# Performance work log

Measured on AMD Instinct MI355X. Metric: run time of the kernel, lower is better.

The kernel has to match this reference:

```python
import jax, jax.numpy as jnp
import numpy as np

BN_EPS = 1e-5


def conv1x1(x, W, b):
    # x: [B, Cin, N], W: [Cout, Cin], b: [Cout]
    return jnp.einsum('bcn,oc->bon', x, W) + b[None, :, None]


def batchnorm(x, gamma, beta):
    # training-mode BatchNorm1d over (batch, spatial) for x: [B, C, N]
    m = jnp.mean(x, axis=(0, 2), keepdims=True)
    v = jnp.var(x, axis=(0, 2), keepdims=True)
    return (x - m) * jax.lax.rsqrt(v + BN_EPS) * gamma[None, :, None] + beta[None, :, None]


def square_distance(a, b):
    # a: [B, N, 3], b: [B, S, 3] -> [B, N, S]
    aa = jnp.sum(a * a, axis=-1, keepdims=True)        # [B,N,1]
    bb = jnp.sum(b * b, axis=-1)[:, None, :]           # [B,1,S]
    return aa + bb - 2.0 * jnp.einsum('bnc,bsc->bns', a, b)


def setup_inputs() -> dict:
    key = jax.random.key(0)
    ks = jax.random.split(key, 16)
    B, N, S = 4, 8192, 2048
    D1, D2 = 128, 256
    Cin, Cout = D1 + D2, 256
    hid = Cout  # res_expansion = 1.0
    inp = {
        'xyz1': jax.random.normal(ks[0], (B, N, 3), jnp.float32),
        'xyz2': jax.random.normal(ks[1], (B, S, 3), jnp.float32),
        'points1': jax.random.normal(ks[2], (B, D1, N), jnp.float32),
        'points2': jax.random.normal(ks[3], (B, D2, S), jnp.float32),
        # fuse: Conv1d(Cin->Cout,k=1) + BN + ReLU
        'W_fuse': jax.random.normal(ks[4], (Cout, Cin), jnp.float32) * (1.0 / np.sqrt(Cin)),
        'b_fuse': jnp.zeros((Cout,), jnp.float32),
        'g_fuse': jnp.ones((Cout,), jnp.float32),
        'be_fuse': jnp.zeros((Cout,), jnp.float32),
        # extraction residual block: conv1 -> bn -> relu -> conv2 -> bn, +res, relu
        'W1': jax.random.normal(ks[5], (hid, Cout), jnp.float32) * (1.0 / np.sqrt(Cout)),
        'b1': jnp.zeros((hid,), jnp.float32),
        'g1': jnp.ones((hid,), jnp.float32),
        'be1': jnp.zeros((hid,), jnp.float32),
        'W2': jax.random.normal(ks[6], (Cout, hid), jnp.float32) * (1.0 / np.sqrt(hid)),
        'b2': jnp.zeros((Cout,), jnp.float32),
        'g2': jnp.ones((Cout,), jnp.float32),
        'be2': jnp.zeros((Cout,), jnp.float32),
    }
    return inp


def reference(xyz1, xyz2, points1, points2,
              W_fuse, b_fuse, g_fuse, be_fuse,
              W1, b1, g1, be1, W2, b2, g2, be2):
    B, N, _ = xyz1.shape
    p2 = jnp.transpose(points2, (0, 2, 1))  # [B, S, D2]
    # 3-NN inverse-distance interpolation
    dists = square_distance(xyz1, xyz2)                 # [B, N, S]
    neg_d3, idx = jax.lax.top_k(-dists, 3)              # 3 smallest distances
    d3 = -neg_d3                                        # [B, N, 3]
    recip = 1.0 / (d3 + 1e-8)
    weight = recip / jnp.sum(recip, axis=2, keepdims=True)  # [B, N, 3]
    gathered = jax.vmap(lambda pts, i: pts[i])(p2, idx)     # [B, N, 3, D2]
    interp = jnp.sum(gathered * weight[..., None], axis=2)  # [B, N, D2]
    # concat skip features
    p1 = jnp.transpose(points1, (0, 2, 1))              # [B, N, D1]
    new_points = jnp.concatenate([p1, interp], axis=-1) # [B, N, D1+D2]
    x = jnp.transpose(new_points, (0, 2, 1))            # [B, Cin, N]
    # fuse: ConvBNReLU1D
    x = jax.nn.relu(batchnorm(conv1x1(x, W_fuse, b_fuse), g_fuse, be_fuse))
    # extraction: residual ConvBNReLURes1D block
    y = jax.nn.relu(batchnorm(conv1x1(x, W1, b1), g1, be1))
    y = batchnorm(conv1x1(y, W2, b2), g2, be2)
    return jax.nn.relu(x + y)
```

## Files before the change

kernel.cpp:

```cpp
#include <hip/hip_runtime.h>
#include <cstdint>
#include <cstddef>

#define B_ 4
#define N_ 8192
#define S_ 2048
#define M_ 32768

typedef short bf16x8 __attribute__((ext_vector_type(8)));
typedef float f32x4 __attribute__((ext_vector_type(4)));

__device__ __forceinline__ float bf2f(unsigned short u) {
  union { unsigned int i; float f; } v; v.i = ((unsigned int)u) << 16; return v.f;
}
__device__ __forceinline__ unsigned short f2bf(float f) {
  union { float f; unsigned int i; } v; v.f = f;
  return (unsigned short)((v.i + 0x7FFFu + ((v.i >> 16) & 1u)) >> 16);
}

__global__ void pack_weights(const float* __restrict__ Wf, const float* __restrict__ W1,
                             const float* __restrict__ W2, unsigned short* __restrict__ out) {
  int i = blockIdx.x * 256 + threadIdx.x;
  float v;
  if (i < 98304)       v = Wf[i];
  else if (i < 163840) v = W1[i - 98304];
  else                 v = W2[i - 163840];
  out[i] = f2bf(v);
}

__global__ void transpose_to_bf16(const float* __restrict__ src, unsigned short* __restrict__ dst,
                                  int C, int Nsp, int ldo, int coff) {
  __shared__ float t[32][33];
  int b = blockIdx.z;
  int n0 = blockIdx.x * 32, c0 = blockIdx.y * 32;
  int x = threadIdx.x, y = threadIdx.y;
  const float* s = src + ((size_t)b * C + c0) * Nsp + n0;
#pragma unroll
  for (int k = 0; k < 4; ++k)
    t[y + k * 8][x] = s[(size_t)(y + k * 8) * Nsp + x];
  __syncthreads();
#pragma unroll
  for (int k = 0; k < 4; ++k) {
    int n = n0 + y + k * 8;
    dst[((size_t)b * Nsp + n) * ldo + coff + c0 + x] = f2bf(t[x][y + k * 8]);
  }
}

__device__ __forceinline__ bool lexlt(float da, int ia, float db, int ib) {
  return (da < db) || (da == db && ia < ib);
}

__global__ __launch_bounds__(256, 8) void knn_interp_kernel(
    const float* __restrict__ xyz1, const float* __restrict__ xyz2,
    const unsigned short* __restrict__ p2t, unsigned short* __restrict__ np) {
  __shared__ float4 sp[1024];
  __shared__ float sw[16][3];
  __shared__ int   sidx[16][3];
  int t = threadIdx.x;
  int b = blockIdx.y;
  const float* xb = xyz2 + (size_t)b * S_ * 3;

  int lane = t & 63, wave = t >> 6;
  int sub = lane & 15;
  int pib = wave * 4 + (lane >> 4);
  int n = blockIdx.x * 16 + pib;
  const float* q = xyz1 + ((size_t)b * N_ + n) * 3;
  float px = q[0], py = q[1], pz = q[2];
  float nx = -2.f * px, ny = -2.f * py, nz = -2.f * pz;
  float aa = fmaf(px, px, fmaf(py, py, pz * pz));

  float d0 = 1e30f, d1 = 1e30f, d2 = 1e30f;
  int i0 = S_, i1 = S_, i2 = S_;

  for (int chunk = 0; chunk < 2; ++chunk) {
    __syncthreads();
    for (int i = t; i < 1024; i += 256) {
      int c = chunk * 1024 + i;
      float cx = xb[3 * c], cy = xb[3 * c + 1], cz = xb[3 * c + 2];
      sp[i] = make_float4(cx, cy, cz, fmaf(cx, cx, fmaf(cy, cy, cz * cz)));
    }
    __syncthreads();
    int sbase = chunk * 1024;
#pragma unroll 4
    for (int i = 0; i < 64; ++i) {
      int sl = i * 16 + sub;
      float4 c = sp[sl];
      float d = fmaf(nx, c.x, fmaf(ny, c.y, fmaf(nz, c.z, c.w)));
      int s = sbase + sl;
      bool b0 = d < d0, b1 = d < d1, b2 = d < d2;
      d2 = b1 ? d1 : (b2 ? d : d2);
      i2 = b1 ? i1 : (b2 ? s : i2);
      d1 = b0 ? d0 : (b1 ? d : d1);
      i1 = b0 ? i0 : (b1 ? s : i1);
      d0 = b0 ? d : d0;
      i0 = b0 ? s : i0;
    }
  }

#pragma unroll
  for (int m = 1; m <= 8; m <<= 1) {
    float e0 = __shfl_xor(d0, m, 64), e1 = __shfl_xor(d1, m, 64), e2 = __shfl_xor(d2, m, 64);
    int   j0 = __shfl_xor(i0, m, 64), j1 = __shfl_xor(i1, m, 64), j2 = __shfl_xor(i2, m, 64);
    bool l0 = lexlt(d0, i0, e0, j0);
    float m0d = l0 ? d0 : e0;  int m0i = l0 ? i0 : j0;
    float x0d = l0 ? e0 : d0;  int x0i = l0 ? j0 : i0;
    bool l11 = lexlt(d1, i1, e1, j1);
    float n1d = l11 ? d1 : e1; int n1i = l11 ? i1 : j1;
    float y1d = l11 ? e1 : d1; int y1i = l11 ? j1 : i1;
    bool l1 = lexlt(n1d, n1i, x0d, x0i);
    float m1d = l1 ? n1d : x0d; int m1i = l1 ? n1i : x0i;
    bool l01 = lexlt(d0, i0, e1, j1);
    float p1d = l01 ? e1 : d0; int p1i = l01 ? j1 : i0;
    bool l10 = lexlt(d1, i1, e0, j0);
    float p2d = l10 ? e0 : d1; int p2i = l10 ? j0 : i1;
    bool lp = lexlt(p1d, p1i, p2d, p2i);
    float p3d = lp ? p1d : p2d; int p3i = lp ? p1i : p2i;
    bool l22 = lexlt(d2, i2, e2, j2);
    float p4d = l22 ? d2 : e2; int p4i = l22 ? i2 : j2;
    bool l2 = lexlt(p3d, p3i, p4d, p4i);
    float m2d = l2 ? p3d : p4d; int m2i = l2 ? p3i : p4i;
    (void)y1d; (void)y1i;
    d0 = m0d; i0 = m0i; d1 = m1d; i1 = m1i; d2 = m2d; i2 = m2i;
  }

  if (sub == 0) {
    float t0 = aa + d0, t1 = aa + d1, t2 = aa + d2;
    float r0 = 1.f / (t0 + 1e-8f), r1 = 1.f / (t1 + 1e-8f), r2 = 1.f / (t2 + 1e-8f);
    float rs = 1.f / (r0 + r1 + r2);
    sw[pib][0] = r0 * rs; sw[pib][1] = r1 * rs; sw[pib][2] = r2 * rs;
    sidx[pib][0] = i0; sidx[pib][1] = i1; sidx[pib][2] = i2;
  }
  __syncthreads();

  for (int p = wave; p < 16; p += 4) {
    float w0 = sw[p][0], w1 = sw[p][1], w2 = sw[p][2];
    const ushort4* g0 = (const ushort4*)(p2t + ((size_t)b * S_ + sidx[p][0]) * 256) + lane;
    const ushort4* g1 = (const ushort4*)(p2t + ((size_t)b * S_ + sidx[p][1]) * 256) + lane;
    const ushort4* g2 = (const ushort4*)(p2t + ((size_t)b * S_ + sidx[p][2]) * 256) + lane;
    ushort4 a = *g0, c = *g1, e = *g2;
    ushort4 o;
    o.x = f2bf(w0 * bf2f(a.x) + w1 * bf2f(c.x) + w2 * bf2f(e.x));
    o.y = f2bf(w0 * bf2f(a.y) + w1 * bf2f(c.y) + w2 * bf2f(e.y));
    o.z = f2bf(w0 * bf2f(a.z) + w1 * bf2f(c.z) + w2 * bf2f(e.z));
    o.w = f2bf(w0 * bf2f(a.w) + w1 * bf2f(c.w) + w2 * bf2f(e.w));
    int nn = blockIdx.x * 16 + p;
    *((ushort4*)(np + ((size_t)b * N_ + nn) * 384 + 128) + lane) = o;
  }
}

__global__ __launch_bounds__(256) void gemm_bt(const unsigned short* __restrict__ A,
                                               const unsigned short* __restrict__ Bw,
                                               float* __restrict__ C, float* __restrict__ sums,
                                               int K) {
  __shared__ unsigned short As[128 * 64];
  __shared__ unsigned short Bs[128 * 64];
  int tid = threadIdx.x;
  int lane = tid & 63, wave = tid >> 6;
  int wr = wave >> 1, wc = wave & 1;
  size_t m0 = (size_t)blockIdx.x * 128;
  int n0 = blockIdx.y * 128;
  int lr = lane & 15, lk = lane >> 4;
  f32x4 acc[4][4] = {};

  for (int kt = 0; kt < K; kt += 64) {
#pragma unroll
    for (int i = 0; i < 4; ++i) {
      int ch = i * 256 + tid;
      int row = ch >> 3;
      int col = (ch & 7) * 8;
      __builtin_amdgcn_global_load_lds(
          (const __attribute__((address_space(1))) void*)(A + (m0 + row) * K + kt + col),
          (__attribute__((address_space(3))) void*)(As + ch * 8), 16, 0, 0);
    }
#pragma unroll
    for (int i = 0; i < 4; ++i) {
      int ch = i * 256 + tid;
      int row = ch >> 3;
      int col = (ch & 7) * 8;
      __builtin_amdgcn_global_load_lds(
          (const __attribute__((address_space(1))) void*)(Bw + (size_t)(n0 + row) * K + kt + col),
          (__attribute__((address_space(3))) void*)(Bs + ch * 8), 16, 0, 0);
    }
    __syncthreads();

    bf16x8 af[4][2], bf[4][2];
#pragma unroll
    for (int m = 0; m < 4; ++m)
#pragma unroll
      for (int kk = 0; kk < 2; ++kk)
        af[m][kk] = *(const bf16x8*)(As + (wr * 64 + m * 16 + lr) * 64 + kk * 32 + lk * 8);
#pragma unroll
    for (int nn = 0; nn < 4; ++nn)
#pragma unroll
      for (int kk = 0; kk < 2; ++kk)
        bf[nn][kk] = *(const bf16x8*)(Bs + (wc * 64 + nn * 16 + lr) * 64 + kk * 32 + lk * 8);

#pragma unroll
    for (int m = 0; m < 4; ++m)
#pragma unroll
      for (int nn = 0; nn < 4; ++nn)
#pragma unroll
        for (int kk = 0; kk < 2; ++kk)
          acc[m][nn] = __builtin_amdgcn_mfma_f32_16x16x32_bf16(af[m][kk], bf[nn][kk], acc[m][nn], 0, 0, 0);
    __syncthreads();
  }

#pragma unroll
  for (int m = 0; m < 4; ++m) {
    size_t row = m0 + wr * 64 + m * 16 + lk * 4;
#pragma unroll
    for (int j = 0; j < 4; ++j) {
      float* cr = C + (row + j) * 256 + n0 + wc * 64 + lr;
#pragma unroll
      for (int nn = 0; nn < 4; ++nn)
        cr[nn * 16] = acc[m][nn][j];
    }
  }

  float cs[4], cq[4];
#pragma unroll
  for (int nn = 0; nn < 4; ++nn) {
    float s = 0.f, qq = 0.f;
#pragma unroll
    for (int m = 0; m < 4; ++m)
#pragma unroll
      for (int j = 0; j < 4; ++j) { float v = acc[m][nn][j]; s += v; qq = fmaf(v, v, qq); }
    cs[nn] = s; cq[nn] = qq;
  }
#pragma unroll
  for (int off = 16; off <= 32; off <<= 1) {
#pragma unroll
    for (int nn = 0; nn < 4; ++nn) {
      cs[nn] += __shfl_xor(cs[nn], off, 64);
      cq[nn] += __shfl_xor(cq[nn], off, 64);
    }
  }
  if (lk == 0) {
#pragma unroll
    for (int nn = 0; nn < 4; ++nn) {
      int c = n0 + wc * 64 + nn * 16 + lr;
      atomicAdd(&sums[c], cs[nn]);
      atomicAdd(&sums[256 + c], cq[nn]);
    }
  }
}

__global__ void bn_relu_kernel(const float* __restrict__ X, const float* __restrict__ sums,
                               const float* __restrict__ g, const float* __restrict__ be,
                               unsigned short* __restrict__ Y) {
  __shared__ float sc[256], sh[256];
  int t = threadIdx.x;
  {
    float s = sums[t], q = sums[256 + t];
    float m = s * (1.0f / 32768.0f);
    float v = q * (1.0f / 32768.0f) - m * m;
    float scale = g[t] * rsqrtf(v + 1e-5f);
    sc[t] = scale; sh[t] = be[t] - m * scale;
  }
  __syncthreads();
  const float4* X4 = (const float4*)X;
  ushort4* Y4 = (ushort4*)Y;
  for (size_t i = (size_t)blockIdx.x * 256 + t; i < (size_t)M_ * 64; i += 2048 * 256) {
    float4 x = X4[i];
    int c0 = (int)((i * 4) & 255);
    ushort4 o;
    o.x = f2bf(fmaxf(x.x * sc[c0 + 0] + sh[c0 + 0], 0.f));
    o.y = f2bf(fmaxf(x.y * sc[c0 + 1] + sh[c0 + 1], 0.f));
    o.z = f2bf(fmaxf(x.z * sc[c0 + 2] + sh[c0 + 2], 0.f));
    o.w = f2bf(fmaxf(x.w * sc[c0 + 3] + sh[c0 + 3], 0.f));
    Y4[i] = o;
  }
}

__global__ void final_kernel(const float* __restrict__ Z, const unsigned short* __restrict__ Xb,
                             const float* __restrict__ sums2, const float* __restrict__ g2,
                             const float* __restrict__ be2, float* __restrict__ out) {
  __shared__ float sc[64], sh[64];
  __shared__ float tile[64 * 65];
  int t = threadIdx.x;
  int o0 = blockIdx.y * 64;
  if (t < 64) {
    int c = o0 + t;
    float s = sums2[c], q = sums2[256 + c];
    float m = s * (1.0f / 32768.0f);
    float v = q * (1.0f / 32768.0f) - m * m;
    float scale = g2[c] * rsqrtf(v + 1e-5f);
    sc[t] = scale; sh[t] = be2[c] - m * scale;
  }
  __syncthreads();
  size_t m0 = (size_t)blockIdx.x * 64;
  int rl = t >> 4, cq = t & 15;
#pragma unroll
  for (int rr = 0; rr < 4; ++rr) {
    int row = rr * 16 + rl;
    size_t base = (m0 + row) * 256 + o0 + cq * 4;
    float4 z = *(const float4*)(Z + base);
    ushort4 x = *(const ushort4*)(Xb + base);
    int c = cq * 4;
    tile[row * 65 + c + 0] = fmaxf(z.x * sc[c + 0] + sh[c + 0] + bf2f(x.x), 0.f);
    tile[row * 65 + c + 1] = fmaxf(z.y * sc[c + 1] + sh[c + 1] + bf2f(x.y), 0.f);
    tile[row * 65 + c + 2] = fmaxf(z.z * sc[c + 2] + sh[c + 2] + bf2f(x.z), 0.f);
    tile[row * 65 + c + 3] = fmaxf(z.w * sc[c + 3] + sh[c + 3] + bf2f(x.w), 0.f);
  }
  __syncthreads();
  int b = (int)(m0 >> 13);
  int nbase = (int)(m0 & 8191);
  int orow = t >> 4, nq = t & 15;
#pragma unroll
  for (int ov = 0; ov < 4; ++ov) {
    int o = ov * 16 + orow;
    float4 v;
    v.x = tile[(nq * 4 + 0) * 65 + o];
    v.y = tile[(nq * 4 + 1) * 65 + o];
    v.z = tile[(nq * 4 + 2) * 65 + o];
    v.w = tile[(nq * 4 + 3) * 65 + o];
    *(float4*)(out + ((size_t)(b * 256 + o0 + o)) * 8192 + nbase + nq * 4) = v;
  }
}

extern "C" void kernel_launch(void* const* d_in, const int* in_sizes, int n_in,
                              void* d_out, int out_size, void* d_ws, size_t ws_size,
                              hipStream_t stream) {
  const float* xyz1    = (const float*)d_in[0];
  const float* xyz2    = (const float*)d_in[1];
  const float* points1 = (const float*)d_in[2];
  const float* points2 = (const float*)d_in[3];
  const float* W_fuse  = (const float*)d_in[4];
  const float* g_fuse  = (const float*)d_in[6];
  const float* be_fuse = (const float*)d_in[7];
  const float* W1      = (const float*)d_in[8];
  const float* g1      = (const float*)d_in[10];
  const float* be1     = (const float*)d_in[11];
  const float* W2      = (const float*)d_in[12];
  const float* g2      = (const float*)d_in[14];
  const float* be2     = (const float*)d_in[15];
  float* out = (float*)d_out;

  char* ws = (char*)d_ws;
  float* lin = (float*)ws;                   ws += (size_t)M_ * 256 * 4;
  unsigned short* xb = (unsigned short*)ws;  ws += (size_t)M_ * 256 * 2;
  unsigned short* np = (unsigned short*)ws;  ws += (size_t)M_ * 384 * 2;
  unsigned short* yb = np;
  unsigned short* p2t = (unsigned short*)ws; ws += (size_t)B_ * S_ * 256 * 2;
  unsigned short* wb = (unsigned short*)ws;  ws += 229376 * 2;
  float* stats = (float*)ws;

  hipMemsetAsync(stats, 0, 6 * 256 * sizeof(float), stream);
  pack_weights<<<896, 256, 0, stream>>>(W_fuse, W1, W2, wb);
  transpose_to_bf16<<<dim3(256, 4, 4), dim3(32, 8), 0, stream>>>(points1, np, 128, N_, 384, 0);
  transpose_to_bf16<<<dim3(64, 8, 4), dim3(32, 8), 0, stream>>>(points2, p2t, 256, S_, 256, 0);
  knn_interp_kernel<<<dim3(N_ / 16, B_), 256, 0, stream>>>(xyz1, xyz2, p2t, np);
  gemm_bt<<<dim3(M_ / 128, 2), 256, 0, stream>>>(np, wb, lin, stats, 384);
  bn_relu_kernel<<<2048, 256, 0, stream>>>(lin, stats, g_fuse, be_fuse, xb);
  gemm_bt<<<dim3(M_ / 128, 2), 256, 0, stream>>>(xb, wb + 98304, lin, stats + 512, 256);
  bn_relu_kernel<<<2048, 256, 0, stream>>>(lin, stats + 512, g1, be1, yb);
  gemm_bt<<<dim3(M_ / 128, 2), 256, 0, stream>>>(yb, wb + 163840, lin, stats + 1024, 256);
  final_kernel<<<dim3(M_ / 64, 4), 256, 0, stream>>>(lin, xb, stats + 1024, g2, be2, out);
}
```

Measured before the change: 183.0 us.

## Restructure KNN as point-per-lane with candidate split across waves; shrink GEMM M tile

The KNN kernel now gives each lane its own query point, and the 8 waves each scan a 256-candidate slice. The slices are read from a precomputed float4 array (coords plus squared norm) built in the prep kernel, which replaces the per-block LDS staging and the shuffle-based merge. The per-wave top-3 lists are merged through shared memory, and the insertion step uses fmed3/fmin for the distances. The GEMM tile is cut from 128 to 64 rows, doubling the number of blocks. In exchange, the broadcast candidate loads go through the global/scalar cache, and the GEMM reuses each B tile over fewer rows.

```diff
diff --git a/kernel.cpp b/kernel.cpp
--- a/kernel.cpp
+++ b/kernel.cpp
@@ -18,14 +18,21 @@
   return (unsigned short)((v.i + 0x7FFFu + ((v.i >> 16) & 1u)) >> 16);
 }
 
-__global__ void pack_weights(const float* __restrict__ Wf, const float* __restrict__ W1,
-                             const float* __restrict__ W2, unsigned short* __restrict__ out) {
+__global__ void prep_kernel(const float* __restrict__ Wf, const float* __restrict__ W1,
+                            const float* __restrict__ W2, unsigned short* __restrict__ wout,
+                            const float* __restrict__ xyz2, float4* __restrict__ c4) {
   int i = blockIdx.x * 256 + threadIdx.x;
-  float v;
-  if (i < 98304)       v = Wf[i];
-  else if (i < 163840) v = W1[i - 98304];
-  else                 v = W2[i - 163840];
-  out[i] = f2bf(v);
+  if (i < 229376) {
+    float v;
+    if (i < 98304)       v = Wf[i];
+    else if (i < 163840) v = W1[i - 98304];
+    else                 v = W2[i - 163840];
+    wout[i] = f2bf(v);
+  } else {
+    int j = i - 229376;
+    float x = xyz2[3 * j], y = xyz2[3 * j + 1], z = xyz2[3 * j + 2];
+    c4[j] = make_float4(x, y, z, fmaf(x, x, fmaf(y, y, z * z)));
+  }
 }
 
 __global__ void transpose_to_bf16(const float* __restrict__ src, unsigned short* __restrict__ dst,
@@ -50,101 +57,87 @@
   return (da < db) || (da == db && ia < ib);
 }
 
-__global__ __launch_bounds__(256, 8) void knn_interp_kernel(
-    const float* __restrict__ xyz1, const float* __restrict__ xyz2,
+__global__ __launch_bounds__(512, 4) void knn_interp_kernel(
+    const float* __restrict__ xyz1, const float4* __restrict__ c4,
     const unsigned short* __restrict__ p2t, unsigned short* __restrict__ np) {
-  __shared__ float4 sp[1024];
-  __shared__ float sw[16][3];
-  __shared__ int   sidx[16][3];
+  __shared__ float sd[8][64][3];
+  __shared__ int   si[8][64][3];
+  __shared__ float sw[64][3];
+  __shared__ int   sidx[64][3];
   int t = threadIdx.x;
-  int b = blockIdx.y;
-  const float* xb = xyz2 + (size_t)b * S_ * 3;
-
   int lane = t & 63, wave = t >> 6;
-  int sub = lane & 15;
-  int pib = wave * 4 + (lane >> 4);
-  int n = blockIdx.x * 16 + pib;
-  const float* q = xyz1 + ((size_t)b * N_ + n) * 3;
+  int g = blockIdx.x * 64 + lane;
+  int b = (blockIdx.x * 64) >> 13;
+  const float* q = xyz1 + (size_t)g * 3;
   float px = q[0], py = q[1], pz = q[2];
-  float nx = -2.f * px, ny = -2.f * py, nz = -2.f * pz;
   float aa = fmaf(px, px, fmaf(py, py, pz * pz));
+  const float4* cb = c4 + ((size_t)b << 11) + (wave << 8);
+  int base = wave << 8;
 
   float d0 = 1e30f, d1 = 1e30f, d2 = 1e30f;
   int i0 = S_, i1 = S_, i2 = S_;
-
-  for (int chunk = 0; chunk < 2; ++chunk) {
-    __syncthreads();
-    for (int i = t; i < 1024; i += 256) {
-      int c = chunk * 1024 + i;
-      float cx = xb[3 * c], cy = xb[3 * c + 1], cz = xb[3 * c + 2];
-      sp[i] = make_float4(cx, cy, cz, fmaf(cx, cx, fmaf(cy, cy, cz * cz)));
-    }
-    __syncthreads();
-    int sbase = chunk * 1024;
-#pragma unroll 4
-    for (int i = 0; i < 64; ++i) {
-      int sl = i * 16 + sub;
-      float4 c = sp[sl];
-      float d = fmaf(nx, c.x, fmaf(ny, c.y, fmaf(nz, c.z, c.w)));
-      int s = sbase + sl;
-      bool b0 = d < d0, b1 = d < d1, b2 = d < d2;
-      d2 = b1 ? d1 : (b2 ? d : d2);
-      i2 = b1 ? i1 : (b2 ? s : i2);
-      d1 = b0 ? d0 : (b1 ? d : d1);
-      i1 = b0 ? i0 : (b1 ? s : i1);
-      d0 = b0 ? d : d0;
-      i0 = b0 ? s : i0;
-    }
-  }
-
-#pragma unroll
-  for (int m = 1; m <= 8; m <<= 1) {
-    float e0 = __shfl_xor(d0, m, 64), e1 = __shfl_xor(d1, m, 64), e2 = __shfl_xor(d2, m, 64);
-    int   j0 = __shfl_xor(i0, m, 64), j1 = __shfl_xor(i1, m, 64), j2 = __shfl_xor(i2, m, 64);
-    bool l0 = lexlt(d0, i0, e0, j0);
-    float m0d = l0 ? d0 : e0;  int m0i = l0 ? i0 : j0;
-    float x0d = l0 ? e0 : d0;  int x0i = l0 ? j0 : i0;
-    bool l11 = lexlt(d1, i1, e1, j1);
-    float n1d = l11 ? d1 : e1; int n1i = l11 ? i1 : j1;
-    float y1d = l11 ? e1 : d1; int y1i = l11 ? j1 : i1;
-    bool l1 = lexlt(n1d, n1i, x0d, x0i);
-    float m1d = l1 ? n1d : x0d; int m1i = l1 ? n1i : x0i;
-    bool l01 = lexlt(d0, i0, e1, j1);
-    float p1d = l01 ? e1 : d0; int p1i = l01 ? j1 : i0;
-    bool l10 = lexlt(d1, i1, e0, j0);
-    float p2d = l10 ? e0 : d1; int p2i = l10 ? j0 : i1;
-    bool lp = lexlt(p1d, p1i, p2d, p2i);
-    float p3d = lp ? p1d : p2d; int p3i = lp ? p1i : p2i;
-    bool l22 = lexlt(d2, i2, e2, j2);
-    float p4d = l22 ? d2 : e2; int p4i = l22 ? i2 : j2;
-    bool l2 = lexlt(p3d, p3i, p4d, p4i);
-    float m2d = l2 ? p3d : p4d; int m2i = l2 ? p3i : p4i;
-    (void)y1d; (void)y1i;
-    d0 = m0d; i0 = m0i; d1 = m1d; i1 = m1i; d2 = m2d; i2 = m2i;
-  }
-
-  if (sub == 0) {
-    float t0 = aa + d0, t1 = aa + d1, t2 = aa + d2;
+  for (int j = 0; j < 256; j += 8) {
+    float4 cc0 = cb[j + 0], cc1 = cb[j + 1], cc2 = cb[j + 2], cc3 = cb[j + 3];
+    float4 cc4 = cb[j + 4], cc5 = cb[j + 5], cc6 = cb[j + 6], cc7 = cb[j + 7];
+#define KNN_INS(CC, U)                                                        \
+    {                                                                         \
+      float dot = fmaf(px, CC.x, fmaf(py, CC.y, pz * CC.z));                  \
+      float d = fmaf(-2.f, dot, CC.w);                     \
+      int s = base + j + U;                                                   \
+      bool b0 = d < d0, b1 = d < d1, b2 = d < d2;                             \
+      i2 = b1 ? i1 : (b2 ? s : i2);                                           \
+      i1 = b0 ? i0 : (b1 ? s : i1);                                           \
+      i0 = b0 ? s : i0;                                                       \
+      float nd1 = __builtin_amdgcn_fmed3f(d, d0, d1);                         \
+      float nd2 = __builtin_amdgcn_fmed3f(d, d1, d2);                         \
+      d0 = fminf(d0, d);                                                      \
+      d1 = nd1; d2 = nd2;                                                     \
+    }
+    KNN_INS(cc0, 0) KNN_INS(cc1, 1) KNN_INS(cc2, 2) KNN_INS(cc3, 3)
+    KNN_INS(cc4, 4) KNN_INS(cc5, 5) KNN_INS(cc6, 6) KNN_INS(cc7, 7)
+#undef KNN_INS
+  }
+  sd[wave][lane][0] = d0; sd[wave][lane][1] = d1; sd[wave][lane][2] = d2;
+  si[wave][lane][0] = i0; si[wave][lane][1] = i1; si[wave][lane][2] = i2;
+  __syncthreads();
+
+  if (t < 64) {
+    float e0 = sd[0][t][0], e1 = sd[0][t][1], e2 = sd[0][t][2];
+    int   j0 = si[0][t][0], j1 = si[0][t][1], j2 = si[0][t][2];
+#pragma unroll
+    for (int w = 1; w < 8; ++w) {
+#pragma unroll
+      for (int k = 0; k < 3; ++k) {
+        float d = sd[w][t][k];
+        int s = si[w][t][k];
+        bool b0 = lexlt(d, s, e0, j0), b1 = lexlt(d, s, e1, j1), b2 = lexlt(d, s, e2, j2);
+        e2 = b1 ? e1 : (b2 ? d : e2);  j2 = b1 ? j1 : (b2 ? s : j2);
+        e1 = b0 ? e0 : (b1 ? d : e1);  j1 = b0 ? j0 : (b1 ? s : j1);
+        e0 = b0 ? d : e0;              j0 = b0 ? s : j0;
+      }
+    }
+    float t0 = aa + e0, t1 = aa + e1, t2 = aa + e2;
     float r0 = 1.f / (t0 + 1e-8f), r1 = 1.f / (t1 + 1e-8f), r2 = 1.f / (t2 + 1e-8f);
     float rs = 1.f / (r0 + r1 + r2);
-    sw[pib][0] = r0 * rs; sw[pib][1] = r1 * rs; sw[pib][2] = r2 * rs;
-    sidx[pib][0] = i0; sidx[pib][1] = i1; sidx[pib][2] = i2;
-  }
-  __syncthreads();
-
-  for (int p = wave; p < 16; p += 4) {
+    sw[t][0] = r0 * rs; sw[t][1] = r1 * rs; sw[t][2] = r2 * rs;
+    sidx[t][0] = j0; sidx[t][1] = j1; sidx[t][2] = j2;
+  }
+  __syncthreads();
+
+  const unsigned short* pb = p2t + ((size_t)b * S_) * 256;
+  for (int p = wave; p < 64; p += 8) {
     float w0 = sw[p][0], w1 = sw[p][1], w2 = sw[p][2];
-    const ushort4* g0 = (const ushort4*)(p2t + ((size_t)b * S_ + sidx[p][0]) * 256) + lane;
-    const ushort4* g1 = (const ushort4*)(p2t + ((size_t)b * S_ + sidx[p][1]) * 256) + lane;
-    const ushort4* g2 = (const ushort4*)(p2t + ((size_t)b * S_ + sidx[p][2]) * 256) + lane;
+    const ushort4* g0 = (const ushort4*)(pb + (size_t)sidx[p][0] * 256) + lane;
+    const ushort4* g1 = (const ushort4*)(pb + (size_t)sidx[p][1] * 256) + lane;
+    const ushort4* g2 = (const ushort4*)(pb + (size_t)sidx[p][2] * 256) + lane;
     ushort4 a = *g0, c = *g1, e = *g2;
     ushort4 o;
     o.x = f2bf(w0 * bf2f(a.x) + w1 * bf2f(c.x) + w2 * bf2f(e.x));
     o.y = f2bf(w0 * bf2f(a.y) + w1 * bf2f(c.y) + w2 * bf2f(e.y));
     o.z = f2bf(w0 * bf2f(a.z) + w1 * bf2f(c.z) + w2 * bf2f(e.z));
     o.w = f2bf(w0 * bf2f(a.w) + w1 * bf2f(c.w) + w2 * bf2f(e.w));
-    int nn = blockIdx.x * 16 + p;
-    *((ushort4*)(np + ((size_t)b * N_ + nn) * 384 + 128) + lane) = o;
+    size_t g2r = (size_t)blockIdx.x * 64 + p;
+    *((ushort4*)(np + g2r * 384 + 128) + lane) = o;
   }
 }
 
@@ -152,19 +145,19 @@
                                                const unsigned short* __restrict__ Bw,
                                                float* __restrict__ C, float* __restrict__ sums,
                                                int K) {
-  __shared__ unsigned short As[128 * 64];
+  __shared__ unsigned short As[64 * 64];
   __shared__ unsigned short Bs[128 * 64];
   int tid = threadIdx.x;
   int lane = tid & 63, wave = tid >> 6;
   int wr = wave >> 1, wc = wave & 1;
-  size_t m0 = (size_t)blockIdx.x * 128;
+  size_t m0 = (size_t)blockIdx.x * 64;
   int n0 = blockIdx.y * 128;
   int lr = lane & 15, lk = lane >> 4;
-  f32x4 acc[4][4] = {};
+  f32x4 acc[2][4] = {};
 
   for (int kt = 0; kt < K; kt += 64) {
 #pragma unroll
-    for (int i = 0; i < 4; ++i) {
+    for (int i = 0; i < 2; ++i) {
       int ch = i * 256 + tid;
       int row = ch >> 3;
       int col = (ch & 7) * 8;
@@ -183,12 +176,12 @@
     }
     __syncthreads();
 
-    bf16x8 af[4][2], bf[4][2];
-#pragma unroll
-    for (int m = 0; m < 4; ++m)
+    bf16x8 af[2][2], bf[4][2];
+#pragma unroll
+    for (int m = 0; m < 2; ++m)
 #pragma unroll
       for (int kk = 0; kk < 2; ++kk)
-        af[m][kk] = *(const bf16x8*)(As + (wr * 64 + m * 16 + lr) * 64 + kk * 32 + lk * 8);
+        af[m][kk] = *(const bf16x8*)(As + (wr * 32 + m * 16 + lr) * 64 + kk * 32 + lk * 8);
 #pragma unroll
     for (int nn = 0; nn < 4; ++nn)
 #pragma unroll
@@ -196,7 +189,7 @@
         bf[nn][kk] = *(const bf16x8*)(Bs + (wc * 64 + nn * 16 + lr) * 64 + kk * 32 + lk * 8);
 
 #pragma unroll
-    for (int m = 0; m < 4; ++m)
+    for (int m = 0; m < 2; ++m)
 #pragma unroll
       for (int nn = 0; nn < 4; ++nn)
 #pragma unroll
@@ -206,8 +199,8 @@
   }
 
 #pragma unroll
-  for (int m = 0; m < 4; ++m) {
-    size_t row = m0 + wr * 64 + m * 16 + lk * 4;
+  for (int m = 0; m < 2; ++m) {
+    size_t row = m0 + wr * 32 + m * 16 + lk * 4;
 #pragma unroll
     for (int j = 0; j < 4; ++j) {
       float* cr = C + (row + j) * 256 + n0 + wc * 64 + lr;
@@ -222,7 +215,7 @@
   for (int nn = 0; nn < 4; ++nn) {
     float s = 0.f, qq = 0.f;
 #pragma unroll
-    for (int m = 0; m < 4; ++m)
+    for (int m = 0; m < 2; ++m)
 #pragma unroll
       for (int j = 0; j < 4; ++j) { float v = acc[m][nn][j]; s += v; qq = fmaf(v, v, qq); }
     cs[nn] = s; cq[nn] = qq;
@@ -343,17 +336,18 @@
   unsigned short* yb = np;
   unsigned short* p2t = (unsigned short*)ws; ws += (size_t)B_ * S_ * 256 * 2;
   unsigned short* wb = (unsigned short*)ws;  ws += 229376 * 2;
+  float4* c4 = (float4*)ws;                  ws += (size_t)B_ * S_ * 16;
   float* stats = (float*)ws;
 
   hipMemsetAsync(stats, 0, 6 * 256 * sizeof(float), stream);
-  pack_weights<<<896, 256, 0, stream>>>(W_fuse, W1, W2, wb);
+  prep_kernel<<<928, 256, 0, stream>>>(W_fuse, W1, W2, wb, xyz2, c4);
   transpose_to_bf16<<<dim3(256, 4, 4), dim3(32, 8), 0, stream>>>(points1, np, 128, N_, 384, 0);
   transpose_to_bf16<<<dim3(64, 8, 4), dim3(32, 8), 0, stream>>>(points2, p2t, 256, S_, 256, 0);
-  knn_interp_kernel<<<dim3(N_ / 16, B_), 256, 0, stream>>>(xyz1, xyz2, p2t, np);
-  gemm_bt<<<dim3(M_ / 128, 2), 256, 0, stream>>>(np, wb, lin, stats, 384);
+  knn_interp_kernel<<<M_ / 64, 512, 0, stream>>>(xyz1, c4, p2t, np);
+  gemm_bt<<<dim3(M_ / 64, 2), 256, 0, stream>>>(np, wb, lin, stats, 384);
   bn_relu_kernel<<<2048, 256, 0, stream>>>(lin, stats, g_fuse, be_fuse, xb);
-  gemm_bt<<<dim3(M_ / 128, 2), 256, 0, stream>>>(xb, wb + 98304, lin, stats + 512, 256);
+  gemm_bt<<<dim3(M_ / 64, 2), 256, 0, stream>>>(xb, wb + 98304, lin, stats + 512, 256);
   bn_relu_kernel<<<2048, 256, 0, stream>>>(lin, stats + 512, g1, be1, yb);
-  gemm_bt<<<dim3(M_ / 128, 2), 256, 0, stream>>>(yb, wb + 163840, lin, stats + 1024, 256);
+  gemm_bt<<<dim3(M_ / 64, 2), 256, 0, stream>>>(yb, wb + 163840, lin, stats + 1024, 256);
   final_kernel<<<dim3(M_ / 64, 4), 256, 0, stream>>>(lin, xb, stats + 1024, g2, be2, out);
 }
```

Result: slower. 239.3 us (+30.7%).
